# Performance work log

Hardware: AMD Instinct MI355X
Metric: run time of the kernel (lower is better)

Reference implementation:

```python
import jax, jax.numpy as jnp
import numpy as np

TAU = 0.5  # config.tau -> ContrastiveLoss temperature


def setup_inputs() -> dict:
    key = jax.random.key(0)
    k1, _ = jax.random.split(key)
    last_hidden_states = jax.random.normal(k1, (256, 512, 768), dtype=jnp.float32)
    input_mask = jnp.ones((256, 512), dtype=jnp.float32)
    return {"last_hidden_states": last_hidden_states, "input_mask": input_mask}


def reference(last_hidden_states, input_mask):
    # --- get_bert_emb with pooling == 'mean' (faithful: sums WITHOUT masking,
    # divides by mask.sum, exactly as the torch code does) ---
    pooled = last_hidden_states.sum(axis=1) / input_mask.sum(axis=-1, keepdims=True)  # [B, H]

    # --- ContrastiveLoss (NT-Xent style, vectorized form of the double loop) ---
    # z = F.normalize(emb_in, dim=1); cosine similarity of normalized rows == z @ z.T
    z = pooled / jnp.linalg.norm(pooled, axis=1, keepdims=True)  # [B, H]
    logits = (z @ z.T) / TAU  # [B, B] similarity_matrix / temperature

    B = logits.shape[0]
    n = B // 4

    # denominator_i = sum_{k != i} exp(S[i,k]/tau)  -> log-domain with diagonal masked
    diag = jnp.eye(B, dtype=bool)
    logden = jax.nn.logsumexp(jnp.where(diag, -jnp.inf, logits), axis=1)  # [B]

    # loss_ij = -log(exp(S[i,j]/tau) / denom_i) = logden[i] - logits[i,j], summed over i<j<n
    pair_mask = jnp.triu(jnp.ones((n, n), dtype=bool), k=1)
    per_pair = logden[:n, None] - logits[:n, :n]  # [n, n]
    total = jnp.sum(jnp.where(pair_mask, per_pair, jnp.zeros_like(per_pair)))

    # final scaling exactly as in the torch code: -2/n * (n-1) * loss
    return -2.0 / n * (n - 1) * total
```

## Files before the change

kernel.cpp:

```cpp
#include <hip/hip_runtime.h>
#include <math.h>

#define B 256
#define S 512
#define H 768
#define H4 (H / 4)
#define NSMALL 64

typedef float f32x4 __attribute__((ext_vector_type(4)));

__device__ __forceinline__ float waveReduceSum(float v) {
    v += __shfl_down(v, 32);
    v += __shfl_down(v, 16);
    v += __shfl_down(v, 8);
    v += __shfl_down(v, 4);
    v += __shfl_down(v, 2);
    v += __shfl_down(v, 1);
    return v;
}

__global__ void pool_z_k(const float* __restrict__ lhs,
                         float* __restrict__ z) {
    const int b = blockIdx.x;
    const int t = threadIdx.x;
    const int col = t % H4;
    const int rg  = t / H4;

    __shared__ f32x4 red[3][H4];
    __shared__ float sq[3];

    const f32x4* __restrict__ src =
        reinterpret_cast<const f32x4*>(lhs) + (size_t)b * S * H4;
    f32x4 acc = {0.f, 0.f, 0.f, 0.f};
#pragma unroll 16
    for (int s = 0; s < S / 4; ++s) {
        f32x4 v = __builtin_nontemporal_load(&src[(size_t)(4 * s + rg) * H4 + col]);
        acc += v;
    }
    if (rg > 0) red[rg - 1][col] = acc;
    __syncthreads();

    if (rg == 0) {
        f32x4 p = acc;
        p += red[0][col];
        p += red[1][col];
        p += red[2][col];
        float s2 = p.x * p.x + p.y * p.y + p.z * p.z + p.w * p.w;
        float ws2 = waveReduceSum(s2);
        if ((t & 63) == 0) sq[t >> 6] = ws2;
        __builtin_amdgcn_s_barrier();
        const float inv_n = 1.0f / sqrtf(sq[0] + sq[1] + sq[2]);
        p *= inv_n;
        reinterpret_cast<f32x4*>(z + (size_t)b * H)[col] = p;
    } else {
        __builtin_amdgcn_s_barrier();
    }
}

__global__ void row_part_k(const float* __restrict__ z,
                           float* __restrict__ sp,
                           float* __restrict__ pairneg) {
    const int i  = blockIdx.x >> 2;
    const int jc = blockIdx.x & 3;
    const int t  = threadIdx.x;
    const int col = t & 63;
    const int q   = t >> 6;
    const int j   = jc * 64 + col;

    __shared__ float zi[H];
    __shared__ float pd[4][64];

    zi[t]       = z[(size_t)i * H + t];
    zi[t + 256] = z[(size_t)i * H + 256 + t];
    zi[t + 512] = z[(size_t)i * H + 512 + t];
    __syncthreads();

    const float4* __restrict__ zj4 =
        reinterpret_cast<const float4*>(z + (size_t)j * H) + q * 48;
    const float4* zi4 = reinterpret_cast<const float4*>(zi) + q * 48;
    float d0 = 0.f, d1 = 0.f;
#pragma unroll 8
    for (int k = 0; k < 48; k += 2) {
        float4 a  = zi4[k];     float4 c1 = zj4[k];
        float4 a2 = zi4[k + 1]; float4 c2 = zj4[k + 1];
        d0 += a.x * c1.x + a.y * c1.y + a.z * c1.z + a.w * c1.w;
        d1 += a2.x * c2.x + a2.y * c2.y + a2.z * c2.z + a2.w * c2.w;
    }
    pd[q][col] = d0 + d1;
    __syncthreads();

    if (t < 64) {
        const float dot = pd[0][t] + pd[1][t] + pd[2][t] + pd[3][t];
        const float logit = dot * 2.0f;
        const float ev = (j == i) ? 0.f : expf(logit);
        float s = waveReduceSum(ev);
        if (t == 0) sp[i * 4 + jc] = s;
        if (jc == 0) {
            const float term = (t > i) ? -logit : 0.f;
            float ts = waveReduceSum(term);
            if (t == 0) pairneg[i] = ts;
        }
    }
}

__global__ void final_k(const float* __restrict__ sp,
                        const float* __restrict__ pairneg,
                        float* __restrict__ out) {
    const int i = threadIdx.x;
    const float s = sp[i * 4] + sp[i * 4 + 1] + sp[i * 4 + 2] + sp[i * 4 + 3];
    const float logden = logf(s);
    const float row = (float)(NSMALL - 1 - i) * logden + pairneg[i];
    float tot = waveReduceSum(row);
    if (i == 0) {
        out[0] = (-2.0f / (float)NSMALL) * (float)(NSMALL - 1) * tot;
    }
}

extern "C" void kernel_launch(void* const* d_in, const int* in_sizes, int n_in,
                              void* d_out, int out_size, void* d_ws, size_t ws_size,
                              hipStream_t stream) {
    const float* lhs  = (const float*)d_in[0];
    float* out = (float*)d_out;
    float* ws  = (float*)d_ws;

    float* z       = ws;
    float* sp      = z + (size_t)B * H;
    float* pairneg = sp + NSMALL * 4;

    pool_z_k<<<B, H, 0, stream>>>(lhs, z);
    row_part_k<<<NSMALL * 4, 256, 0, stream>>>(z, sp, pairneg);
    final_k<<<1, 64, 0, stream>>>(sp, pairneg, out);
}
```

Baseline: 73.64 us.

## Split sequence pooling across four blocks per batch row with separate normalize kernel

The mean-pool reduction over the 512-token sequence is split into four quarter-sequence blocks per batch row, so 1024 blocks stream the input instead of 256. Partial sums go to a workspace buffer, and a new small kernel adds the four partials and L2-normalizes each row. This aims to fill more compute units and keep more memory requests in flight for the bandwidth-bound pass over the 400MB input. The cost is an extra kernel launch and a small partial-sum write and read.

```diff
diff --git a/kernel.cpp b/kernel.cpp
--- a/kernel.cpp
+++ b/kernel.cpp
@@ -5,6 +5,8 @@
 #define S 512
 #define H 768
 #define H4 (H / 4)
+#define NQ 4
+#define QROWS (S / NQ)
 #define NSMALL 64
 
 typedef float f32x4 __attribute__((ext_vector_type(4)));
@@ -19,21 +21,23 @@
     return v;
 }
 
-__global__ void pool_z_k(const float* __restrict__ lhs,
-                         float* __restrict__ z) {
-    const int b = blockIdx.x;
-    const int t = threadIdx.x;
+__global__ void pool_partial_k(const float* __restrict__ lhs,
+                               f32x4* __restrict__ part) {
+    const int blk = blockIdx.x;
+    const int b   = blk >> 2;
+    const int qq  = blk & 3;
+    const int t   = threadIdx.x;
     const int col = t % H4;
     const int rg  = t / H4;
 
     __shared__ f32x4 red[3][H4];
-    __shared__ float sq[3];
 
     const f32x4* __restrict__ src =
-        reinterpret_cast<const f32x4*>(lhs) + (size_t)b * S * H4;
+        reinterpret_cast<const f32x4*>(lhs) +
+        ((size_t)b * S + (size_t)qq * QROWS) * H4;
     f32x4 acc = {0.f, 0.f, 0.f, 0.f};
 #pragma unroll 16
-    for (int s = 0; s < S / 4; ++s) {
+    for (int s = 0; s < QROWS / 4; ++s) {
         f32x4 v = __builtin_nontemporal_load(&src[(size_t)(4 * s + rg) * H4 + col]);
         acc += v;
     }
@@ -45,16 +49,29 @@
         p += red[0][col];
         p += red[1][col];
         p += red[2][col];
-        float s2 = p.x * p.x + p.y * p.y + p.z * p.z + p.w * p.w;
-        float ws2 = waveReduceSum(s2);
-        if ((t & 63) == 0) sq[t >> 6] = ws2;
-        __builtin_amdgcn_s_barrier();
-        const float inv_n = 1.0f / sqrtf(sq[0] + sq[1] + sq[2]);
-        p *= inv_n;
-        reinterpret_cast<f32x4*>(z + (size_t)b * H)[col] = p;
-    } else {
-        __builtin_amdgcn_s_barrier();
+        part[((size_t)qq * B + b) * H4 + col] = p;
     }
+}
+
+__global__ void pool_norm_k(const f32x4* __restrict__ part,
+                            float* __restrict__ z) {
+    const int b = blockIdx.x;
+    const int t = threadIdx.x;
+
+    __shared__ float sq[3];
+
+    f32x4 p = part[((size_t)0 * B + b) * H4 + t];
+    p += part[((size_t)1 * B + b) * H4 + t];
+    p += part[((size_t)2 * B + b) * H4 + t];
+    p += part[((size_t)3 * B + b) * H4 + t];
+
+    float s2 = p.x * p.x + p.y * p.y + p.z * p.z + p.w * p.w;
+    float ws2 = waveReduceSum(s2);
+    if ((t & 63) == 0) sq[t >> 6] = ws2;
+    __syncthreads();
+    const float inv_n = 1.0f / sqrtf(sq[0] + sq[1] + sq[2]);
+    p *= inv_n;
+    reinterpret_cast<f32x4*>(z + (size_t)b * H)[t] = p;
 }
 
 __global__ void row_part_k(const float* __restrict__ z,
@@ -123,11 +140,13 @@
     float* out = (float*)d_out;
     float* ws  = (float*)d_ws;
 
-    float* z       = ws;
+    f32x4* part    = (f32x4*)ws;
+    float* z       = ws + (size_t)NQ * B * H;
     float* sp      = z + (size_t)B * H;
     float* pairneg = sp + NSMALL * 4;
 
-    pool_z_k<<<B, H, 0, stream>>>(lhs, z);
+    pool_partial_k<<<B * NQ, H, 0, stream>>>(lhs, part);
+    pool_norm_k<<<B, H4, 0, stream>>>(part, z);
     row_part_k<<<NSMALL * 4, 256, 0, stream>>>(z, sp, pairneg);
     final_k<<<1, 64, 0, stream>>>(sp, pairneg, out);
 }
```

Measured after the change: 77.95 us. 5.9% more time.
